# Kernel tuning notes

Measured on AMD Instinct MI355X. Metric: run time of the kernel, lower is better.

Reference implementation:

```python
import jax, jax.numpy as jnp
import numpy as np

BLANK = 512            # blank_idx = vocab_size
DURATIONS = (1, 2, 3, 4)
SIGMA = 0.05           # logit under-normalization weight
NEG = -1e30            # safe -inf (keeps gradients finite)


def setup_inputs() -> dict:
    key = jax.random.key(0)
    k1, k2, k3 = jax.random.split(key, 3)
    B, T, U, V = 8, 256, 64, 512
    D = len(DURATIONS)
    label_acts = jax.random.normal(k1, (B, T, U + 1, V + 1), dtype=jnp.float32)
    duration_acts = jax.random.normal(k2, (B, T, U + 1, D), dtype=jnp.float32)
    targets = jax.random.randint(k3, (B, U), 0, V, dtype=jnp.int32)
    input_lengths = jnp.full((B,), T, dtype=jnp.int32)
    target_lengths = jnp.full((B,), U, dtype=jnp.int32)
    return {"label_acts": label_acts, "duration_acts": duration_acts,
            "targets": targets, "input_lengths": input_lengths,
            "target_lengths": target_lengths}


def _lag(x, d):
    # x: [T, ...] -> y with y[t] = x[t - d], NEG-padded at the front
    pad = jnp.full_like(x[:d], NEG)
    return jnp.concatenate([pad, x[: x.shape[0] - d]], axis=0)


def _tdt_loglike(label_acts, duration_acts, targets, input_lengths, target_lengths):
    B, T, U1, _ = label_acts.shape
    U = U1 - 1
    D = len(DURATIONS)

    lp = jax.nn.log_softmax(label_acts, axis=-1) - SIGMA        # [B,T,U+1,V+1]
    lpb = lp[..., BLANK]                                         # [B,T,U+1] blank logp
    lpy = jnp.take_along_axis(                                   # [B,T,U] target-label logp
        lp[:, :, :U, :], targets[:, None, :, None].astype(jnp.int32), axis=3
    )[..., 0]
    ld = jax.nn.log_softmax(duration_acts, axis=-1)              # [B,T,U+1,D]

    # time-major views for the scan
    lpb_t = jnp.transpose(lpb, (1, 0, 2))                        # [T,B,U+1]
    lpy_t = jnp.transpose(lpy, (1, 0, 2))                        # [T,B,U]
    ld_t = jnp.transpose(ld, (1, 0, 2, 3))                       # [T,B,U+1,D]

    # lagged emission terms: entry at scan step t is the value at t - duration
    lb_lag = jnp.stack([_lag(lpb_t, d) for d in DURATIONS], axis=1)                       # [T,D,B,U+1]
    ly_lag = jnp.stack([_lag(lpy_t, d) for d in DURATIONS], axis=1)                       # [T,D,B,U]
    ld_lag = jnp.stack([_lag(ld_t[..., i], d) for i, d in enumerate(DURATIONS)], axis=1)  # [T,D,B,U+1]

    dmax = max(DURATIONS)
    alpha0 = jnp.concatenate(
        [jnp.zeros((B, 1), jnp.float32), jnp.full((B, U), NEG, jnp.float32)], axis=1)     # [B,U+1]
    hist0 = jnp.concatenate(
        [alpha0[None], jnp.full((dmax - 1, B, U1), NEG, jnp.float32)], axis=0)            # [dmax,B,U+1]

    def step(hist, xs):
        # hist[a] = alpha[t-1-a]
        lb, ly, ldr = xs  # [D,B,U+1], [D,B,U], [D,B,U+1]
        blank_terms = jnp.stack([hist[d - 1] + lb[i] + ldr[i]
                                 for i, d in enumerate(DURATIONS)])      # [D,B,U+1]
        blank_in = jax.nn.logsumexp(blank_terms, axis=0)                 # [B,U+1]
        label_terms = jnp.stack([hist[d - 1][:, :U] + ly[i] + ldr[i][:, :U]
                                 for i, d in enumerate(DURATIONS)])      # [D,B,U]
        label_in = jax.nn.logsumexp(label_terms, axis=0)                 # [B,U]
        alpha_t = jnp.concatenate(
            [blank_in[:, :1], jnp.logaddexp(blank_in[:, 1:], label_in)], axis=1)
        hist = jnp.concatenate([alpha_t[None], hist[:-1]], axis=0)
        return hist, alpha_t

    _, alphas_rest = jax.lax.scan(step, hist0, (lb_lag[1:], ly_lag[1:], ld_lag[1:]))
    alphas = jnp.concatenate([alpha0[None], alphas_rest], axis=0)        # [T,B,U+1]

    # final: from (T_b - d, U_b) emit blank with duration d landing exactly at T_b
    dur = jnp.asarray(DURATIONS, jnp.int32)                              # [D]
    t_idx = input_lengths[:, None].astype(jnp.int32) - dur[None, :]      # [B,D]
    valid = t_idx >= 0
    t_safe = jnp.clip(t_idx, 0, T - 1)
    b_idx = jnp.arange(B)[:, None]
    u_idx = target_lengths[:, None].astype(jnp.int32)
    a_fin = alphas[t_safe, b_idx, u_idx]                                 # [B,D]
    lpb_fin = lpb[b_idx, t_safe, u_idx]                                  # [B,D]
    ld_fin = ld[b_idx, t_safe, u_idx, jnp.arange(D)[None, :]]            # [B,D]
    terms = jnp.where(valid, a_fin + lpb_fin + ld_fin, NEG)
    return jax.nn.logsumexp(terms, axis=1)                               # [B] log-likelihood


def reference(label_acts, duration_acts, targets, input_lengths, target_lengths):
    ll = _tdt_loglike(label_acts, duration_acts, targets, input_lengths, target_lengths)
    return jnp.mean(-ll)  # reduction='mean'
```

## Files before the change

### kernel.cpp

```cpp
#include <hip/hip_runtime.h>

#define TDT_B  8
#define TDT_T  256
#define TDT_U  64
#define TDT_U1 65
#define TDT_V1 513
#define TP     275
#define SIG    0.05f
#define SHIFT  3.0f

#define OFF_PYD (TDT_B * TP * TDT_U1 * 4)

__global__ __launch_bounds__(256) void k_prep(
    const float* __restrict__ la, const float* __restrict__ da,
    const int* __restrict__ tgt, float* __restrict__ ws,
    float* __restrict__ out)
{
  if (blockIdx.x == 0 && threadIdx.x == 0) out[0] = 0.f;

  const int l = threadIdx.x & 63;
  const int r = (blockIdx.x << 2) + (threadIdx.x >> 6);
  const int u  = r % TDT_U1;
  const int bt = r / TDT_U1;
  const int t  = bt & (TDT_T - 1);
  const int b  = bt >> 8;

  const float* row = la + (size_t)r * TDT_V1;
  const int ofs = r & 1;
  const float2* p2 = (const float2*)(row + ofs);
  float2 w[4];
#pragma unroll
  for (int k = 0; k < 4; ++k) w[k] = p2[l + (k << 6)];
  const float extra = row[ofs ? 0 : 512];

  float m = extra;
#pragma unroll
  for (int k = 0; k < 4; ++k) m = fmaxf(m, fmaxf(w[k].x, w[k].y));
#pragma unroll
  for (int off = 32; off; off >>= 1) m = fmaxf(m, __shfl_xor(m, off));
  float s = (l == 0) ? __expf(extra - m) : 0.f;
#pragma unroll
  for (int k = 0; k < 4; ++k) s += __expf(w[k].x - m) + __expf(w[k].y - m);
#pragma unroll
  for (int off = 32; off; off >>= 1) s += __shfl_xor(s, off);
  const float lse = m + __logf(s);

  const float4 dv = *(const float4*)(da + ((size_t)r << 2));
  const float m4 = fmaxf(fmaxf(dv.x, dv.y), fmaxf(dv.z, dv.w));
  const float l4 = m4 + __logf(__expf(dv.x - m4) + __expf(dv.y - m4) +
                               __expf(dv.z - m4) + __expf(dv.w - m4));
  const float d0 = dv.x - l4 + SHIFT * 1.0f;
  const float d1 = dv.y - l4 + SHIFT * 2.0f;
  const float d2 = dv.z - l4 + SHIFT * 3.0f;
  const float d3 = dv.w - l4 + SHIFT * 4.0f;

  float4* WB4 = (float4*)ws;
  float4* WY4 = (float4*)(ws + OFF_PYD);

  const int tp = t + 4;
  const float xb = ofs ? w[3].y : extra;
  if (l == (ofs ? 63 : 0)) {
    const float pb = xb - lse - SIG;
    WB4[(b * TP + tp) * TDT_U1 + u] =
        make_float4(__expf(pb + d0), __expf(pb + d1), __expf(pb + d2), __expf(pb + d3));
  }

  const int tg = (u < TDT_U) ? tgt[b * TDT_U + u] : -1;
  bool own = false; float vt = 0.f;
#pragma unroll
  for (int k = 0; k < 4; ++k) {
    const int base = ofs + ((l + (k << 6)) << 1);
    if (base == tg)     { vt = w[k].x; own = true; }
    if (base + 1 == tg) { vt = w[k].y; own = true; }
  }
  if (ofs && tg == 0 && l == 0) { vt = extra; own = true; }
  if (own) {
    const float py = vt - lse - SIG;
    WY4[(b * TP + tp) * TDT_U + u] =
        make_float4(__expf(py + d0), __expf(py + d1), __expf(py + d2), __expf(py + d3));
  }

  if (t < 4 && l == 0) {
    const float4 z4 = make_float4(0.f, 0.f, 0.f, 0.f);
    WB4[(b * TP + t) * TDT_U1 + u] = z4;
    if (u < TDT_U) WY4[(b * TP + t) * TDT_U + u] = z4;
  }
}

__device__ __forceinline__ float shup1(float x) {
  const int r = __builtin_amdgcn_update_dpp(
      0, __float_as_int(x), 0x138, 0xf, 0xf, true);
  return __int_as_float(r);
}

__global__ __launch_bounds__(64, 1) void k_dp(
    const float* __restrict__ ws, float* __restrict__ out)
{
  const int b = blockIdx.x;
  const int l = threadIdx.x;
  const float4* WB4p = (const float4*)ws + (size_t)b * (TP * TDT_U1);
  const float4* WY4p = (const float4*)(ws + OFF_PYD) + (size_t)b * (TP * TDT_U);

  __shared__ float4 gl[TP];
  for (int i = l; i < TP; i += 64) gl[i] = WB4p[i * TDT_U1 + 64];
  __syncthreads();

  float4 B0,B1,B2,B3,B4,B5,B6,B7,B8,B9,B10,B11,B12,B13,B14;
  float4 Y0,Y1,Y2,Y3,Y4,Y5,Y6,Y7,Y8,Y9,Y10,Y11,Y12,Y13,Y14;
  float4 G0,G1,G2,G3,G4,G5,G6,G7,G8,G9,G10,G11,G12,G13,G14;

#define LOADSLOT(S, tpi) do {                \
    const int _tp = (tpi);                   \
    B##S = WB4p[_tp * TDT_U1 + l];           \
    Y##S = WY4p[_tp * TDT_U  + l];           \
    G##S = gl[_tp];                          \
  } while (0)

  LOADSLOT(1, 1);  LOADSLOT(2, 2);  LOADSLOT(3, 3);  LOADSLOT(4, 4);
  LOADSLOT(5, 5);  LOADSLOT(6, 6);  LOADSLOT(7, 7);  LOADSLOT(8, 8);
  LOADSLOT(9, 9);  LOADSLOT(10,10); LOADSLOT(11,11); LOADSLOT(12,12);
  LOADSLOT(13,13); LOADSLOT(14,14); LOADSLOT(0, 15);

  float a1 = (l == 0) ? 1.f : 0.f, a2 = 0.f, a3 = 0.f, a4 = 0.f;
  float c1 = 0.f, c2 = 0.f, c3 = 0.f, c4 = 0.f;
  float L = 0.f;

#define STEP(S0,S1,S2,S3, TPL) do {                                          \
    float ly0 = a1 * Y##S0.x, ly1 = a2 * Y##S1.y,                            \
          ly2 = a3 * Y##S2.z, ly3 = a4 * Y##S3.w;                            \
    float m0 = shup1(ly0), m1 = shup1(ly1),                                  \
          m2 = shup1(ly2), m3 = shup1(ly3);                                  \
    float cnew = c1*G##S0.x + c2*G##S1.y + c3*G##S2.z + c4*G##S3.w           \
               + ((ly0 + ly1) + (ly2 + ly3));                                \
    float anew = a1*B##S0.x + a2*B##S1.y + a3*B##S2.z + a4*B##S3.w           \
               + ((m0 + m1) + (m2 + m3));                                    \
    a4 = a3; a3 = a2; a2 = a1; a1 = anew;                                    \
    c4 = c3; c3 = c2; c2 = c1; c1 = cnew;                                    \
    LOADSLOT(S3, TPL);                                                       \
  } while (0)

  for (int tb = 1; tb < 256; tb += 15) {
    if (tb != 1) {
      const float r1 = __shfl(a1, tb >> 3);
      const float r2 = __shfl(a1, tb >> 2);
      const float rl = fmaxf(r1, r2);
      const float sc = (rl > 1e-30f) ? (1.0f / rl) : 1.0f;
      L -= __logf(sc);
      a1 *= sc; a2 *= sc; a3 *= sc; a4 *= sc;
      c1 *= sc; c2 *= sc; c3 *= sc; c4 *= sc;
    }
    STEP(4,3,2,1,    tb + 15);
    STEP(5,4,3,2,    tb + 16);
    STEP(6,5,4,3,    tb + 17);
    STEP(7,6,5,4,    tb + 18);
    STEP(8,7,6,5,    tb + 19);
    STEP(9,8,7,6,    tb + 20);
    STEP(10,9,8,7,   tb + 21);
    STEP(11,10,9,8,  tb + 22);
    STEP(12,11,10,9, tb + 23);
    STEP(13,12,11,10,tb + 24);
    STEP(14,13,12,11,tb + 25);
    STEP(0,14,13,12, tb + 26);
    STEP(1,0,14,13,  tb + 27);
    STEP(2,1,0,14,   tb + 28);
    STEP(3,2,1,0,    tb + 29);
  }

  if (l == 63) {
    const float sum = c1 * gl[259].x
                    + c2 * gl[258].y
                    + c3 * gl[257].z
                    + c4 * gl[256].w;
    const float ll = L - SHIFT * 256.0f + __logf(sum);
    atomicAdd(out, ll * (-1.0f / TDT_B));
  }
#undef STEP
#undef LOADSLOT
}

extern "C" void kernel_launch(void* const* d_in, const int* in_sizes, int n_in,
                              void* d_out, int out_size, void* d_ws, size_t ws_size,
                              hipStream_t stream)
{
  const float* la = (const float*)d_in[0];
  const float* da = (const float*)d_in[1];
  const int*   tg = (const int*)d_in[2];
  float* ws  = (float*)d_ws;
  float* out = (float*)d_out;

  const int rows = TDT_B * TDT_T * TDT_U1;
  k_prep<<<rows / 4, 256, 0, stream>>>(la, da, tg, ws, out);
  k_dp  <<<TDT_B, 64, 0, stream>>>(ws, out);
}
```

Measured before the change: 82.11 us.

## Warp-specialize DP kernel with producer waves staging tiles into LDS ring

The DP kernel now runs 256 threads per batch. Three producer waves prefetch the next 15-timestep group of blank and label weights from global memory into a double-buffered shared-memory ring, while wave 0 runs the recurrence by reading from LDS. The aim is to take global-load latency off the serial DP critical path. In exchange it adds a block barrier per group and uses a large shared buffer.

```diff
diff --git a/kernel.cpp b/kernel.cpp
--- a/kernel.cpp
+++ b/kernel.cpp
@@ -9,7 +9,7 @@
 #define SIG    0.05f
 #define SHIFT  3.0f
 
-#define OFF_PYD (TDT_B * TP * TDT_U1 * 4)
+#define OFF_PYD 572000
 
 __global__ __launch_bounds__(256) void k_prep(
     const float* __restrict__ la, const float* __restrict__ da,
@@ -93,39 +93,64 @@
   return __int_as_float(r);
 }
 
-__global__ __launch_bounds__(64, 1) void k_dp(
+__device__ __forceinline__ void fill_group(
+    const float4* __restrict__ WB4p, const float4* __restrict__ WY4p,
+    float4* ring, int j, int wv, int l)
+{
+  const int sb = 15 * j + wv;
+  const int rb = 15 * (j & 1) + (wv - 1);
+#pragma unroll
+  for (int k = 0; k < 5; ++k) {
+    const int s    = sb + 3 * k;
+    const int slot = rb + 3 * k;
+    const float4* sB = WB4p + (size_t)s * TDT_U1;
+    const float4* sY = WY4p + (size_t)s * TDT_U;
+    const float4 vb = sB[l];
+    const float4 vy = sY[l];
+    ring[slot * 130 + l]      = vb;
+    ring[slot * 130 + 65 + l] = vy;
+    if (l == 0) ring[slot * 130 + 64] = sB[64];
+  }
+}
+
+__global__ __launch_bounds__(256, 1) void k_dp(
     const float* __restrict__ ws, float* __restrict__ out)
 {
-  const int b = blockIdx.x;
-  const int l = threadIdx.x;
+  const int b  = blockIdx.x;
+  const int wv = threadIdx.x >> 6;
+  const int l  = threadIdx.x & 63;
   const float4* WB4p = (const float4*)ws + (size_t)b * (TP * TDT_U1);
   const float4* WY4p = (const float4*)(ws + OFF_PYD) + (size_t)b * (TP * TDT_U);
 
-  __shared__ float4 gl[TP];
-  for (int i = l; i < TP; i += 64) gl[i] = WB4p[i * TDT_U1 + 64];
+  __shared__ float4 ring_s[30 * 130];
+  float4* ring = ring_s;
+
+  if (wv != 0) fill_group(WB4p, WY4p, ring, 0, wv, l);
   __syncthreads();
 
   float4 B0,B1,B2,B3,B4,B5,B6,B7,B8,B9,B10,B11,B12,B13,B14;
   float4 Y0,Y1,Y2,Y3,Y4,Y5,Y6,Y7,Y8,Y9,Y10,Y11,Y12,Y13,Y14;
   float4 G0,G1,G2,G3,G4,G5,G6,G7,G8,G9,G10,G11,G12,G13,G14;
-
-#define LOADSLOT(S, tpi) do {                \
-    const int _tp = (tpi);                   \
-    B##S = WB4p[_tp * TDT_U1 + l];           \
-    Y##S = WY4p[_tp * TDT_U  + l];           \
-    G##S = gl[_tp];                          \
-  } while (0)
-
-  LOADSLOT(1, 1);  LOADSLOT(2, 2);  LOADSLOT(3, 3);  LOADSLOT(4, 4);
-  LOADSLOT(5, 5);  LOADSLOT(6, 6);  LOADSLOT(7, 7);  LOADSLOT(8, 8);
-  LOADSLOT(9, 9);  LOADSLOT(10,10); LOADSLOT(11,11); LOADSLOT(12,12);
-  LOADSLOT(13,13); LOADSLOT(14,14); LOADSLOT(0, 15);
-
-  float a1 = (l == 0) ? 1.f : 0.f, a2 = 0.f, a3 = 0.f, a4 = 0.f;
+  float a1 = 0.f, a2 = 0.f, a3 = 0.f, a4 = 0.f;
   float c1 = 0.f, c2 = 0.f, c3 = 0.f, c4 = 0.f;
   float L = 0.f;
 
-#define STEP(S0,S1,S2,S3, TPL) do {                                          \
+#define LOADSLOT(S, RS) do {                 \
+    const int _rb4 = (RS) * 130;             \
+    B##S = ring[_rb4 + l];                   \
+    Y##S = ring[_rb4 + 65 + l];              \
+    G##S = ring[_rb4 + 64];                  \
+  } while (0)
+
+  if (wv == 0) {
+    LOADSLOT(1, 0);  LOADSLOT(2, 1);  LOADSLOT(3, 2);  LOADSLOT(4, 3);
+    LOADSLOT(5, 4);  LOADSLOT(6, 5);  LOADSLOT(7, 6);  LOADSLOT(8, 7);
+    LOADSLOT(9, 8);  LOADSLOT(10,9);  LOADSLOT(11,10); LOADSLOT(12,11);
+    LOADSLOT(13,12); LOADSLOT(14,13); LOADSLOT(0, 14);
+    a1 = (l == 0) ? 1.f : 0.f;
+  }
+
+#define STEP(S0,S1,S2,S3, RSL) do {                                          \
     float ly0 = a1 * Y##S0.x, ly1 = a2 * Y##S1.y,                            \
           ly2 = a3 * Y##S2.z, ly3 = a4 * Y##S3.w;                            \
     float m0 = shup1(ly0), m1 = shup1(ly1),                                  \
@@ -136,41 +161,46 @@
                + ((m0 + m1) + (m2 + m3));                                    \
     a4 = a3; a3 = a2; a2 = a1; a1 = anew;                                    \
     c4 = c3; c3 = c2; c2 = c1; c1 = cnew;                                    \
-    LOADSLOT(S3, TPL);                                                       \
+    LOADSLOT(S3, RSL);                                                       \
   } while (0)
 
-  for (int tb = 1; tb < 256; tb += 15) {
-    if (tb != 1) {
-      const float r1 = __shfl(a1, tb >> 3);
-      const float r2 = __shfl(a1, tb >> 2);
-      const float rl = fmaxf(r1, r2);
-      const float sc = (rl > 1e-30f) ? (1.0f / rl) : 1.0f;
-      L -= __logf(sc);
-      a1 *= sc; a2 *= sc; a3 *= sc; a4 *= sc;
-      c1 *= sc; c2 *= sc; c3 *= sc; c4 *= sc;
+  for (int i = 0, tb = 1; i < 17; ++i, tb += 15) {
+    if (wv != 0) fill_group(WB4p, WY4p, ring, i + 1, wv, l);
+    __syncthreads();
+    if (wv == 0) {
+      const int rb = 15 * ((i + 1) & 1);
+      if (i) {
+        const float r1 = __shfl(a1, tb >> 3);
+        const float r2 = __shfl(a1, tb >> 2);
+        const float rl = fmaxf(r1, r2);
+        const float sc = (rl > 1e-30f) ? (1.0f / rl) : 1.0f;
+        L -= __logf(sc);
+        a1 *= sc; a2 *= sc; a3 *= sc; a4 *= sc;
+        c1 *= sc; c2 *= sc; c3 *= sc; c4 *= sc;
+      }
+      STEP(4,3,2,1,    rb + 0);
+      STEP(5,4,3,2,    rb + 1);
+      STEP(6,5,4,3,    rb + 2);
+      STEP(7,6,5,4,    rb + 3);
+      STEP(8,7,6,5,    rb + 4);
+      STEP(9,8,7,6,    rb + 5);
+      STEP(10,9,8,7,   rb + 6);
+      STEP(11,10,9,8,  rb + 7);
+      STEP(12,11,10,9, rb + 8);
+      STEP(13,12,11,10,rb + 9);
+      STEP(14,13,12,11,rb + 10);
+      STEP(0,14,13,12, rb + 11);
+      STEP(1,0,14,13,  rb + 12);
+      STEP(2,1,0,14,   rb + 13);
+      STEP(3,2,1,0,    rb + 14);
     }
-    STEP(4,3,2,1,    tb + 15);
-    STEP(5,4,3,2,    tb + 16);
-    STEP(6,5,4,3,    tb + 17);
-    STEP(7,6,5,4,    tb + 18);
-    STEP(8,7,6,5,    tb + 19);
-    STEP(9,8,7,6,    tb + 20);
-    STEP(10,9,8,7,   tb + 21);
-    STEP(11,10,9,8,  tb + 22);
-    STEP(12,11,10,9, tb + 23);
-    STEP(13,12,11,10,tb + 24);
-    STEP(14,13,12,11,tb + 25);
-    STEP(0,14,13,12, tb + 26);
-    STEP(1,0,14,13,  tb + 27);
-    STEP(2,1,0,14,   tb + 28);
-    STEP(3,2,1,0,    tb + 29);
-  }
-
-  if (l == 63) {
-    const float sum = c1 * gl[259].x
-                    + c2 * gl[258].y
-                    + c3 * gl[257].z
-                    + c4 * gl[256].w;
+  }
+
+  if (wv == 0 && l == 63) {
+    const float sum = c1 * ring[18 * 130 + 64].x
+                    + c2 * ring[17 * 130 + 64].y
+                    + c3 * ring[16 * 130 + 64].z
+                    + c4 * ring[15 * 130 + 64].w;
     const float ll = L - SHIFT * 256.0f + __logf(sum);
     atomicAdd(out, ll * (-1.0f / TDT_B));
   }
@@ -190,5 +220,5 @@
 
   const int rows = TDT_B * TDT_T * TDT_U1;
   k_prep<<<rows / 4, 256, 0, stream>>>(la, da, tg, ws, out);
-  k_dp  <<<TDT_B, 64, 0, stream>>>(ws, out);
-}
+  k_dp  <<<TDT_B, 256, 0, stream>>>(ws, out);
+}
```

After: 100.5 us. 1.22x slower.
